# Optimization experiments

Hardware: AMD Instinct MI355X
Metric: run time of the kernel (lower is better)

## Reference

```python
import jax, jax.numpy as jnp
import numpy as np

D_MODEL = 1024
N_HEADS = 16
D_HEAD = D_MODEL // N_HEADS


def setup_inputs() -> dict:
    key = jax.random.key(0)
    ks = jax.random.split(key, 9)
    s = 1.0 / np.sqrt(D_MODEL)
    def lin(kw, kb):
        W = jax.random.uniform(kw, (D_MODEL, D_MODEL), jnp.float32, -s, s)
        b = jax.random.uniform(kb, (D_MODEL,), jnp.float32, -s, s)
        return W, b
    Wq, bq = lin(ks[0], ks[1])
    Wk, bk = lin(ks[2], ks[3])
    Wv, bv = lin(ks[4], ks[5])
    Wo, bo = lin(ks[6], ks[7])
    x = jax.random.normal(ks[8], (4, 2048, D_MODEL), jnp.float32)
    return {"x": x, "Wq": Wq, "bq": bq, "Wk": Wk, "bk": bk,
            "Wv": Wv, "bv": bv, "Wo": Wo, "bo": bo}


def reference(x, Wq, bq, Wk, bk, Wv, bv, Wo, bo):
    B, T, C = x.shape
    # torch Linear: y = x @ W.T + b
    Q = x @ Wq.T + bq
    K = x @ Wk.T + bk
    V = x @ Wv.T + bv
    # [B, H, T, Dh]
    Q = Q.reshape(B, T, N_HEADS, D_HEAD).transpose(0, 2, 1, 3)
    K = K.reshape(B, T, N_HEADS, D_HEAD).transpose(0, 2, 1, 3)
    V = V.reshape(B, T, N_HEADS, D_HEAD).transpose(0, 2, 1, 3)
    scale = jnp.float32(np.sqrt(D_HEAD))
    scores = jnp.einsum('bhqd,bhkd->bhqk', Q, K) / scale
    causal = jnp.tril(jnp.ones((T, T), dtype=bool))  # True where allowed
    scores = jnp.where(causal, scores, jnp.float32(-jnp.inf))
    attn = jax.nn.softmax(scores, axis=-1)
    out = jnp.einsum('bhqk,bhkd->bhqd', attn, V)
    out = out.transpose(0, 2, 1, 3).reshape(B, T, C)
    return out @ Wo.T + bo
```

## Files before the change

### kernel.cpp

```cpp
#include <hip/hip_runtime.h>
#include <hip/hip_bf16.h>


typedef float f32x4 __attribute__((ext_vector_type(4)));
typedef __bf16 bf16x8 __attribute__((ext_vector_type(8)));

#define DEVI __device__ __forceinline__

#define QSCALE 0.1803368801111204f

template<int N> struct IC { static constexpr int value = N; };

DEVI ushort f2b(float x) {
  __hip_bfloat16 h = __float2bfloat16(x);
  return __builtin_bit_cast(ushort, h);
}

DEVI unsigned int pkbf(float a, float b) {
#if __has_builtin(__builtin_amdgcn_cvt_pk_bf16_f32)
  typedef __bf16 bf16x2 __attribute__((ext_vector_type(2)));
  bf16x2 r = __builtin_amdgcn_cvt_pk_bf16_f32(a, b);
  return __builtin_bit_cast(unsigned int, r);
#else
  return (unsigned int)f2b(a) | ((unsigned int)f2b(b) << 16);
#endif
}

DEVI bf16x8 ldsFrag(const ushort* p) {
  return __builtin_bit_cast(bf16x8, *(const uint4*)p);
}

DEVI f32x4 mfma16(bf16x8 a, bf16x8 b, f32x4 c) {
  return __builtin_amdgcn_mfma_f32_16x16x32_bf16(a, b, c, 0, 0, 0);
}

DEVI void gload_lds16(const ushort* g, ushort* l) {
  __builtin_amdgcn_global_load_lds(
      (const __attribute__((address_space(1))) unsigned int*)g,
      (__attribute__((address_space(3))) unsigned int*)l, 16, 0, 0);
}

__global__ void k_cvt(const float4* __restrict__ in, ushort4* __restrict__ out, int n4) {
  int i = blockIdx.x * 256 + threadIdx.x;
  if (i >= n4) return;
  float4 f = in[i];
  ushort4 o;
  o.x = f2b(f.x); o.y = f2b(f.y); o.z = f2b(f.z); o.w = f2b(f.w);
  out[i] = o;
}

__global__ void k_cvtW(const float4* __restrict__ w0, const float4* __restrict__ w1,
                       const float4* __restrict__ w2, const float4* __restrict__ w3,
                       ushort4* __restrict__ out) {
  const int y = blockIdx.y;
  const float4* src = (y == 0) ? w0 : (y == 1) ? w1 : (y == 2) ? w2 : w3;
  const int i = blockIdx.x * 256 + threadIdx.x;
  float4 f = src[i];
  ushort4 o;
  o.x = f2b(f.x); o.y = f2b(f.y); o.z = f2b(f.z); o.w = f2b(f.w);
  out[y * 262144 + i] = o;
}

template<int MODE>
__global__ __launch_bounds__(256)
void k_gemm(const ushort* __restrict__ A, const ushort* __restrict__ W,
            const float* __restrict__ b0, const float* __restrict__ b1,
            const float* __restrict__ b2, float* __restrict__ outF,
            ushort* __restrict__ oQ, ushort* __restrict__ oK, ushort* __restrict__ oV) {
  __shared__ ushort As[128 * 32];
  __shared__ ushort Bs[128 * 32];
  const int tid = threadIdx.x;
  const int wave = tid >> 6, lane = tid & 63;
  const int col = lane & 15, quad = lane >> 4;
  const int id = blockIdx.x;
  const int s_ = id >> 3;
  const int m0 = ((id & 7) * 8 + (s_ & 7)) * 128;
  const int n0 = (s_ >> 3) * 128;
  const int wm = (wave >> 1) * 64, wn = (wave & 1) * 64;
  f32x4 acc[4][4] = {};

  const int srow = wave * 16 + (lane >> 2);
  const int scol = (lane & 3) * 8;
  const ushort* Ag = A + (m0 + srow) * 1024 + scol;
  const ushort* Wg = W + (n0 + srow) * 1024 + scol;
  ushort* AsBase0 = &As[(wave * 16) * 32];
  ushort* AsBase1 = &As[(64 + wave * 16) * 32];
  ushort* BsBase0 = &Bs[(wave * 16) * 32];
  ushort* BsBase1 = &Bs[(64 + wave * 16) * 32];

  const int matId = (MODE == 0) ? (n0 >> 10) : 0;

  auto kloop = [&](auto swc) {
    constexpr bool SW = (decltype(swc)::value != 0);
    for (int k0 = 0; k0 < 1024; k0 += 32) {
      __syncthreads();
      gload_lds16(Ag + k0,             AsBase0);
      gload_lds16(Ag + 64 * 1024 + k0, AsBase1);
      gload_lds16(Wg + k0,             BsBase0);
      gload_lds16(Wg + 64 * 1024 + k0, BsBase1);
      __syncthreads();

      bf16x8 af[4], bfr[4];
#pragma unroll
      for (int i = 0; i < 4; ++i)
        af[i] = ldsFrag(&As[(wm + i * 16 + col) * 32 + quad * 8]);
#pragma unroll
      for (int j = 0; j < 4; ++j)
        bfr[j] = ldsFrag(&Bs[(wn + j * 16 + col) * 32 + quad * 8]);
#pragma unroll
      for (int i = 0; i < 4; ++i)
#pragma unroll
        for (int j = 0; j < 4; ++j) {
          if constexpr (SW)
            acc[i][j] = mfma16(bfr[j], af[i], acc[i][j]);
          else
            acc[i][j] = mfma16(af[i], bfr[j], acc[i][j]);
        }
    }
  };

  if (MODE == 1 || matId < 2) kloop(IC<1>{}); else kloop(IC<0>{});

  if (MODE == 1) {
#pragma unroll
    for (int j = 0; j < 4; ++j) {
      const int nb = n0 + wn + j * 16 + quad * 4;
      const float4 bb = *(const float4*)&b0[nb];
#pragma unroll
      for (int i = 0; i < 4; ++i) {
        const int m = m0 + wm + i * 16 + col;
        float4 v;
        v.x = acc[i][j][0] + bb.x;
        v.y = acc[i][j][1] + bb.y;
        v.z = acc[i][j][2] + bb.z;
        v.w = acc[i][j][3] + bb.w;
        *(float4*)&outF[(size_t)m * 1024 + nb] = v;
      }
    }
  } else if (matId < 2) {
    ushort* dst = (matId == 0) ? oQ : oK;
    const float* bias = (matId == 0) ? b0 : b1;
    const float sc = (matId == 0) ? QSCALE : 1.0f;
#pragma unroll
    for (int j = 0; j < 4; ++j) {
      const int nl = ((n0 & 1023) + wn + j * 16 + quad * 4);
      const int h = nl >> 6, dh0 = nl & 63;
      const float4 bb = *(const float4*)&bias[nl];
#pragma unroll
      for (int i = 0; i < 4; ++i) {
        const int m = m0 + wm + i * 16 + col;
        const int b = m >> 11, t = m & 2047;
        ushort4 pk;
        pk.x = f2b((acc[i][j][0] + bb.x) * sc);
        pk.y = f2b((acc[i][j][1] + bb.y) * sc);
        pk.z = f2b((acc[i][j][2] + bb.z) * sc);
        pk.w = f2b((acc[i][j][3] + bb.w) * sc);
        *(ushort4*)&dst[(((size_t)(b * 16 + h) * 2048) + t) * 64 + dh0] = pk;
      }
    }
  } else {
#pragma unroll
    for (int j = 0; j < 4; ++j) {
      const int nl = ((n0 & 1023) + wn + j * 16 + col);
      const int h = nl >> 6, dh = nl & 63;
      const float bn = b2[nl];
#pragma unroll
      for (int i = 0; i < 4; ++i) {
        const int mBase = m0 + wm + i * 16 + quad * 4;
        const int b = mBase >> 11, t = mBase & 2047;
        ushort4 pk;
        pk.x = f2b(acc[i][j][0] + bn);
        pk.y = f2b(acc[i][j][1] + bn);
        pk.z = f2b(acc[i][j][2] + bn);
        pk.w = f2b(acc[i][j][3] + bn);
        *(ushort4*)&oV[(((size_t)(b * 16 + h) * 64) + dh) * 2048 + t] = pk;
      }
    }
  }
}

__global__ __launch_bounds__(256, 2)
void k_attn(const ushort* __restrict__ Q, const ushort* __restrict__ K,
            const ushort* __restrict__ Vt, ushort* __restrict__ AO) {
  __shared__ ushort Ks[2 * 4096];
  __shared__ ushort Vs[2 * 4096];
  __shared__ ushort Os[512];
  __shared__ ushort Ps[4 * 2 * 16 * 72];
  const int tid = threadIdx.x;
  const int wave = tid >> 6, lane = tid & 63;
  const int col = lane & 15, quad = lane >> 4;
  const int id = blockIdx.x;
  const int bh = (id & 7) * 8 + ((id >> 3) & 7);
  const int pr = id >> 6;
  const ushort* Qg = Q + (size_t)bh * 2048 * 64;
  const ushort* Kg = K + (size_t)bh * 2048 * 64;
  const ushort* Vg = Vt + (size_t)bh * 64 * 2048;

  if (tid < 128) {
    const ushort one = 0x3F80;
    ushort4 zv;
    if (tid < 8) { zv.x = one; zv.y = one; zv.z = one; zv.w = one; }
    else         { zv.x = 0;   zv.y = 0;   zv.z = 0;   zv.w = 0;   }
    *(ushort4*)&Os[tid * 4] = zv;
  }

  const int srow = wave * 16 + (lane >> 2);
  const int scol = (lane & 3) * 8;
  ushort* Pw0 = &Ps[((wave * 2 + 0) * 16 + col) * 72];
  ushort* Pw1 = &Ps[((wave * 2 + 1) * 16 + col) * 72];

  for (int pp = 0; pp < 2; ++pp) {
    const int t = pp ? (15 - pr) : pr;
    const int q0 = t * 128;

    bf16x8 qf[2][2];
#pragma unroll
    for (int s = 0; s < 2; ++s) {
      const ushort* p = Qg + (q0 + wave * 32 + s * 16 + col) * 64 + quad * 8;
      qf[s][0] = __builtin_bit_cast(bf16x8, *(const uint4*)p);
      qf[s][1] = __builtin_bit_cast(bf16x8, *(const uint4*)(p + 32));
    }

    f32x4 o[2][4] = {};
    f32x4 la[2] = {};

    const ushort* kPtr = Kg + srow * 64 + scol;
    const ushort* vPtr = Vg + srow * 2048 + scol;

    auto stage = [&](auto bufc) {
      constexpr int BUF = decltype(bufc)::value;
      ushort* kb = &Ks[BUF * 4096 + (wave * 16) * 32];
      ushort* vb = &Vs[BUF * 4096 + (wave * 16) * 32];
      gload_lds16(kPtr,      kb);
      gload_lds16(kPtr + 32, kb + 2048);
      gload_lds16(vPtr,      vb);
      gload_lds16(vPtr + 32, vb + 2048);
      kPtr += 64 * 64;
      vPtr += 64;
    };

    auto step = [&](auto bufc, auto maskc, int j0) {
      constexpr int BUF = decltype(bufc)::value;
      constexpr bool MASKED = (decltype(maskc)::value != 0);
      const ushort* Kb = &Ks[BUF * 4096];
      const ushort* Vb = &Vs[BUF * 4096];
      bf16x8 kf[4][2];
#pragma unroll
      for (int i = 0; i < 4; ++i) {
        kf[i][0] = ldsFrag(&Kb[(i * 16 + col) * 32 + quad * 8]);
        kf[i][1] = ldsFrag(&Kb[(64 + i * 16 + col) * 32 + quad * 8]);
      }
#pragma unroll
      for (int s = 0; s < 2; ++s) {
        ushort* Pw = s ? Pw1 : Pw0;
        const int dlim = MASKED ? (q0 + wave * 32 + s * 16 + col - j0 - quad * 4) : 0;
#pragma unroll
        for (int i = 0; i < 4; ++i) {
          f32x4 z = {0.f, 0.f, 0.f, 0.f};
          f32x4 sv = mfma16(kf[i][0], qf[s][0], z);
          sv = mfma16(kf[i][1], qf[s][1], sv);
          if (MASKED) {
#pragma unroll
            for (int r = 0; r < 4; ++r)
              if (i * 16 + r > dlim) sv[r] = -1e30f;
          }
          f32x4 pv;
#pragma unroll
          for (int r = 0; r < 4; ++r) pv[r] = __builtin_amdgcn_exp2f(sv[r]);
          uint2 pk;
          pk.x = pkbf(pv[0], pv[1]);
          pk.y = pkbf(pv[2], pv[3]);
          *(uint2*)&Pw[i * 16 + quad * 4] = pk;
        }
      }
      bf16x8 osf = ldsFrag(&Os[col * 32 + quad * 8]);
#pragma unroll
      for (int c = 0; c < 2; ++c) {
        bf16x8 pb0 = ldsFrag(&Pw0[c * 32 + quad * 8]);
        bf16x8 pb1 = ldsFrag(&Pw1[c * 32 + quad * 8]);
        la[0] = mfma16(osf, pb0, la[0]);
        la[1] = mfma16(osf, pb1, la[1]);
#pragma unroll
        for (int i = 0; i < 4; ++i) {
          bf16x8 vf = ldsFrag(&Vb[c * 2048 + (i * 16 + col) * 32 + quad * 8]);
          o[0][i] = mfma16(vf, pb0, o[0][i]);
          o[1][i] = mfma16(vf, pb1, o[1][i]);
        }
      }
    };

    __syncthreads();
    stage(IC<0>{});
    for (int it2 = 0; it2 < t; ++it2) {
      __syncthreads();
      stage(IC<1>{});
      step(IC<0>{}, IC<0>{}, 0);
      __syncthreads();
      stage(IC<0>{});
      step(IC<1>{}, IC<0>{}, 0);
    }
    __syncthreads();
    stage(IC<1>{});
    step(IC<0>{}, IC<1>{}, q0);
    __syncthreads();
    step(IC<1>{}, IC<1>{}, q0 + 64);

    const float invs[2] = {1.0f / __shfl(la[0][0], col), 1.0f / __shfl(la[1][0], col)};
    const int b = bh >> 4, h = bh & 15;
#pragma unroll
    for (int s = 0; s < 2; ++s) {
      const float inv = invs[s];
      const int tq = q0 + wave * 32 + s * 16 + col;
      ushort* dst = AO + (size_t)(b * 2048 + tq) * 1024 + h * 64;
#pragma unroll
      for (int i = 0; i < 4; ++i) {
        f32x4 v = o[s][i];
        ushort4 pk;
        pk.x = f2b(v[0] * inv);
        pk.y = f2b(v[1] * inv);
        pk.z = f2b(v[2] * inv);
        pk.w = f2b(v[3] * inv);
        *(ushort4*)&dst[i * 16 + quad * 4] = pk;
      }
    }
  }
}

extern "C" void kernel_launch(void* const* d_in, const int* in_sizes, int n_in,
                              void* d_out, int out_size, void* d_ws, size_t ws_size,
                              hipStream_t stream) {
  const float* x  = (const float*)d_in[0];
  const float* Wq = (const float*)d_in[1];
  const float* bq = (const float*)d_in[2];
  const float* Wk = (const float*)d_in[3];
  const float* bk = (const float*)d_in[4];
  const float* Wv = (const float*)d_in[5];
  const float* bv = (const float*)d_in[6];
  const float* Wo = (const float*)d_in[7];
  const float* bo = (const float*)d_in[8];
  float* out = (float*)d_out;

  char* ws = (char*)d_ws;
  ushort* xb    = (ushort*)ws;
  ushort* Wcat  = (ushort*)(ws + (size_t)16 * 1024 * 1024);
  ushort* Wob   = Wcat + (size_t)3 * 1024 * 1024;
  ushort* Qh    = (ushort*)(ws + (size_t)24 * 1024 * 1024);
  ushort* Kh    = Qh + (size_t)8192 * 1024;
  ushort* Vt    = Kh + (size_t)8192 * 1024;
  ushort* AO    = Vt + (size_t)8192 * 1024;

  k_cvt<<<8192, 256, 0, stream>>>((const float4*)x, (ushort4*)xb, 8192 * 1024 / 4);
  k_cvtW<<<dim3(1024, 4), 256, 0, stream>>>((const float4*)Wq, (const float4*)Wk,
                                            (const float4*)Wv, (const float4*)Wo,
                                            (ushort4*)Wcat);

  k_gemm<0><<<1536, 256, 0, stream>>>(xb, Wcat, bq, bk, bv, nullptr, Qh, Kh, Vt);

  k_attn<<<512, 256, 0, stream>>>(Qh, Kh, Vt, AO);

  k_gemm<1><<<512, 256, 0, stream>>>(AO, Wob, bo, nullptr, nullptr, out,
                                     nullptr, nullptr, nullptr);
}
```

Baseline: 262.8 us.

## Swizzle LDS tiles with BK=64 in GEMM and split attention into per-tile blocks

The GEMM now stages 64-wide K slices into LDS using an XOR-swizzled row layout, which halves the number of barriers per K loop and avoids LDS bank conflicts on fragment reads. The attention kernel uses the same swizzled 64-column K/V layout. It also launches one block per query tile instead of pairing two tiles per block, with an interleaved tile order to balance the causal work. Occupancy hints rise to three blocks per CU. GEMM LDS use doubles and the attention kernel loses the balanced pairing, so more blocks have uneven causal lengths.

After: 253.7 us. 3.5% less time.

```diff
diff --git a/kernel.cpp b/kernel.cpp
--- a/kernel.cpp
+++ b/kernel.cpp
@@ -67,8 +67,8 @@
             const float* __restrict__ b0, const float* __restrict__ b1,
             const float* __restrict__ b2, float* __restrict__ outF,
             ushort* __restrict__ oQ, ushort* __restrict__ oK, ushort* __restrict__ oV) {
-  __shared__ ushort As[128 * 32];
-  __shared__ ushort Bs[128 * 32];
+  __shared__ ushort As[128 * 64];
+  __shared__ ushort Bs[128 * 64];
   const int tid = threadIdx.x;
   const int wave = tid >> 6, lane = tid & 63;
   const int col = lane & 15, quad = lane >> 4;
@@ -79,43 +79,45 @@
   const int wm = (wave >> 1) * 64, wn = (wave & 1) * 64;
   f32x4 acc[4][4] = {};
 
-  const int srow = wave * 16 + (lane >> 2);
-  const int scol = (lane & 3) * 8;
-  const ushort* Ag = A + (m0 + srow) * 1024 + scol;
-  const ushort* Wg = W + (n0 + srow) * 1024 + scol;
-  ushort* AsBase0 = &As[(wave * 16) * 32];
-  ushort* AsBase1 = &As[(64 + wave * 16) * 32];
-  ushort* BsBase0 = &Bs[(wave * 16) * 32];
-  ushort* BsBase1 = &Bs[(64 + wave * 16) * 32];
+  const int grow = lane >> 3;
+  const int gchunk = ((lane & 7) ^ grow) * 8;
+  const ushort* Ag = A + (size_t)(m0 + wave * 8 + grow) * 1024 + gchunk;
+  const ushort* Wg = W + (size_t)(n0 + wave * 8 + grow) * 1024 + gchunk;
+  ushort* AsW = &As[wave * 512];
+  ushort* BsW = &Bs[wave * 512];
 
   const int matId = (MODE == 0) ? (n0 >> 10) : 0;
+  const int cswz = col & 7;
 
   auto kloop = [&](auto swc) {
     constexpr bool SW = (decltype(swc)::value != 0);
-    for (int k0 = 0; k0 < 1024; k0 += 32) {
+    for (int k0 = 0; k0 < 1024; k0 += 64) {
       __syncthreads();
-      gload_lds16(Ag + k0,             AsBase0);
-      gload_lds16(Ag + 64 * 1024 + k0, AsBase1);
-      gload_lds16(Wg + k0,             BsBase0);
-      gload_lds16(Wg + 64 * 1024 + k0, BsBase1);
+#pragma unroll
+      for (int g = 0; g < 4; ++g) {
+        gload_lds16(Ag + (size_t)g * 32 * 1024 + k0, AsW + g * 2048);
+        gload_lds16(Wg + (size_t)g * 32 * 1024 + k0, BsW + g * 2048);
+      }
       __syncthreads();
-
-      bf16x8 af[4], bfr[4];
-#pragma unroll
-      for (int i = 0; i < 4; ++i)
-        af[i] = ldsFrag(&As[(wm + i * 16 + col) * 32 + quad * 8]);
-#pragma unroll
-      for (int j = 0; j < 4; ++j)
-        bfr[j] = ldsFrag(&Bs[(wn + j * 16 + col) * 32 + quad * 8]);
-#pragma unroll
-      for (int i = 0; i < 4; ++i)
-#pragma unroll
-        for (int j = 0; j < 4; ++j) {
-          if constexpr (SW)
-            acc[i][j] = mfma16(bfr[j], af[i], acc[i][j]);
-          else
-            acc[i][j] = mfma16(af[i], bfr[j], acc[i][j]);
-        }
+#pragma unroll
+      for (int kk = 0; kk < 2; ++kk) {
+        bf16x8 af[4], bfr[4];
+#pragma unroll
+        for (int i = 0; i < 4; ++i)
+          af[i] = ldsFrag(&As[(wm + i * 16 + col) * 64 + (((kk * 4 + quad) ^ cswz) * 8)]);
+#pragma unroll
+        for (int j = 0; j < 4; ++j)
+          bfr[j] = ldsFrag(&Bs[(wn + j * 16 + col) * 64 + (((kk * 4 + quad) ^ cswz) * 8)]);
+#pragma unroll
+        for (int i = 0; i < 4; ++i)
+#pragma unroll
+          for (int j = 0; j < 4; ++j) {
+            if constexpr (SW)
+              acc[i][j] = mfma16(bfr[j], af[i], acc[i][j]);
+            else
+              acc[i][j] = mfma16(af[i], bfr[j], acc[i][j]);
+          }
+      }
     }
   };
 
@@ -179,7 +181,7 @@
   }
 }
 
-__global__ __launch_bounds__(256, 2)
+__global__ __launch_bounds__(256, 3)
 void k_attn(const ushort* __restrict__ Q, const ushort* __restrict__ K,
             const ushort* __restrict__ Vt, ushort* __restrict__ AO) {
   __shared__ ushort Ks[2 * 4096];
@@ -191,7 +193,10 @@
   const int col = lane & 15, quad = lane >> 4;
   const int id = blockIdx.x;
   const int bh = (id & 7) * 8 + ((id >> 3) & 7);
-  const int pr = id >> 6;
+  const int tt = id >> 6;
+  const int hi = tt >> 2, lo = tt & 3;
+  const int t = (hi & 1) ? (15 - (hi >> 1) - 2 * lo) : ((hi >> 1) + 2 * lo);
+  const int q0 = t * 128;
   const ushort* Qg = Q + (size_t)bh * 2048 * 64;
   const ushort* Kg = K + (size_t)bh * 2048 * 64;
   const ushort* Vg = Vt + (size_t)bh * 64 * 2048;
@@ -204,124 +209,119 @@
     *(ushort4*)&Os[tid * 4] = zv;
   }
 
-  const int srow = wave * 16 + (lane >> 2);
-  const int scol = (lane & 3) * 8;
+  bf16x8 qf[2][2];
+#pragma unroll
+  for (int s = 0; s < 2; ++s) {
+    const ushort* p = Qg + (q0 + wave * 32 + s * 16 + col) * 64 + quad * 8;
+    qf[s][0] = __builtin_bit_cast(bf16x8, *(const uint4*)p);
+    qf[s][1] = __builtin_bit_cast(bf16x8, *(const uint4*)(p + 32));
+  }
+
+  f32x4 o[2][4] = {};
+  f32x4 la[2] = {};
+
+  const int grow = lane >> 3;
+  const int gchunk = ((lane & 7) ^ grow) * 8;
+  const ushort* kPtr = Kg + (wave * 8 + grow) * 64 + gchunk;
+  const ushort* vPtr = Vg + (size_t)(wave * 8 + grow) * 2048 + gchunk;
   ushort* Pw0 = &Ps[((wave * 2 + 0) * 16 + col) * 72];
   ushort* Pw1 = &Ps[((wave * 2 + 1) * 16 + col) * 72];
-
-  for (int pp = 0; pp < 2; ++pp) {
-    const int t = pp ? (15 - pr) : pr;
-    const int q0 = t * 128;
-
-    bf16x8 qf[2][2];
+  const int cswz = col & 7;
+
+  auto stage = [&](auto bufc) {
+    constexpr int BUF = decltype(bufc)::value;
+    ushort* kb = &Ks[BUF * 4096 + wave * 512];
+    ushort* vb = &Vs[BUF * 4096 + wave * 512];
+    gload_lds16(kPtr,             kb);
+    gload_lds16(kPtr + 32 * 64,   kb + 2048);
+    gload_lds16(vPtr,             vb);
+    gload_lds16(vPtr + 32 * 2048, vb + 2048);
+    kPtr += 64 * 64;
+    vPtr += 64;
+  };
+
+  auto step = [&](auto bufc, auto maskc, int j0) {
+    constexpr int BUF = decltype(bufc)::value;
+    constexpr bool MASKED = (decltype(maskc)::value != 0);
+    const ushort* Kb = &Ks[BUF * 4096];
+    const ushort* Vb = &Vs[BUF * 4096];
+    bf16x8 kf[4][2];
+#pragma unroll
+    for (int i = 0; i < 4; ++i) {
+      kf[i][0] = ldsFrag(&Kb[(i * 16 + col) * 64 + (((0 * 4 + quad) ^ cswz) * 8)]);
+      kf[i][1] = ldsFrag(&Kb[(i * 16 + col) * 64 + (((1 * 4 + quad) ^ cswz) * 8)]);
+    }
 #pragma unroll
     for (int s = 0; s < 2; ++s) {
-      const ushort* p = Qg + (q0 + wave * 32 + s * 16 + col) * 64 + quad * 8;
-      qf[s][0] = __builtin_bit_cast(bf16x8, *(const uint4*)p);
-      qf[s][1] = __builtin_bit_cast(bf16x8, *(const uint4*)(p + 32));
-    }
-
-    f32x4 o[2][4] = {};
-    f32x4 la[2] = {};
-
-    const ushort* kPtr = Kg + srow * 64 + scol;
-    const ushort* vPtr = Vg + srow * 2048 + scol;
-
-    auto stage = [&](auto bufc) {
-      constexpr int BUF = decltype(bufc)::value;
-      ushort* kb = &Ks[BUF * 4096 + (wave * 16) * 32];
-      ushort* vb = &Vs[BUF * 4096 + (wave * 16) * 32];
-      gload_lds16(kPtr,      kb);
-      gload_lds16(kPtr + 32, kb + 2048);
-      gload_lds16(vPtr,      vb);
-      gload_lds16(vPtr + 32, vb + 2048);
-      kPtr += 64 * 64;
-      vPtr += 64;
-    };
-
-    auto step = [&](auto bufc, auto maskc, int j0) {
-      constexpr int BUF = decltype(bufc)::value;
-      constexpr bool MASKED = (decltype(maskc)::value != 0);
-      const ushort* Kb = &Ks[BUF * 4096];
-      const ushort* Vb = &Vs[BUF * 4096];
-      bf16x8 kf[4][2];
-#pragma unroll
-      for (int i = 0; i < 4; ++i) {
-        kf[i][0] = ldsFrag(&Kb[(i * 16 + col) * 32 + quad * 8]);
-        kf[i][1] = ldsFrag(&Kb[(64 + i * 16 + col) * 32 + quad * 8]);
-      }
-#pragma unroll
-      for (int s = 0; s < 2; ++s) {
-        ushort* Pw = s ? Pw1 : Pw0;
-        const int dlim = MASKED ? (q0 + wave * 32 + s * 16 + col - j0 - quad * 4) : 0;
-#pragma unroll
-        for (int i = 0; i < 4; ++i) {
-          f32x4 z = {0.f, 0.f, 0.f, 0.f};
-          f32x4 sv = mfma16(kf[i][0], qf[s][0], z);
-          sv = mfma16(kf[i][1], qf[s][1], sv);
-          if (MASKED) {
-#pragma unroll
-            for (int r = 0; r < 4; ++r)
-              if (i * 16 + r > dlim) sv[r] = -1e30f;
-          }
-          f32x4 pv;
-#pragma unroll
-          for (int r = 0; r < 4; ++r) pv[r] = __builtin_amdgcn_exp2f(sv[r]);
-          uint2 pk;
-          pk.x = pkbf(pv[0], pv[1]);
-          pk.y = pkbf(pv[2], pv[3]);
-          *(uint2*)&Pw[i * 16 + quad * 4] = pk;
+      ushort* Pw = s ? Pw1 : Pw0;
+      const int dlim = MASKED ? (q0 + wave * 32 + s * 16 + col - j0 - quad * 4) : 0;
+#pragma unroll
+      for (int i = 0; i < 4; ++i) {
+        f32x4 z = {0.f, 0.f, 0.f, 0.f};
+        f32x4 sv = mfma16(kf[i][0], qf[s][0], z);
+        sv = mfma16(kf[i][1], qf[s][1], sv);
+        if (MASKED) {
+#pragma unroll
+          for (int r = 0; r < 4; ++r)
+            if (i * 16 + r > dlim) sv[r] = -1e30f;
         }
-      }
-      bf16x8 osf = ldsFrag(&Os[col * 32 + quad * 8]);
-#pragma unroll
-      for (int c = 0; c < 2; ++c) {
-        bf16x8 pb0 = ldsFrag(&Pw0[c * 32 + quad * 8]);
-        bf16x8 pb1 = ldsFrag(&Pw1[c * 32 + quad * 8]);
-        la[0] = mfma16(osf, pb0, la[0]);
-        la[1] = mfma16(osf, pb1, la[1]);
-#pragma unroll
-        for (int i = 0; i < 4; ++i) {
-          bf16x8 vf = ldsFrag(&Vb[c * 2048 + (i * 16 + col) * 32 + quad * 8]);
-          o[0][i] = mfma16(vf, pb0, o[0][i]);
-          o[1][i] = mfma16(vf, pb1, o[1][i]);
-        }
-      }
-    };
-
+        f32x4 pv;
+#pragma unroll
+        for (int r = 0; r < 4; ++r) pv[r] = __builtin_amdgcn_exp2f(sv[r]);
+        uint2 pk;
+        pk.x = pkbf(pv[0], pv[1]);
+        pk.y = pkbf(pv[2], pv[3]);
+        *(uint2*)&Pw[i * 16 + quad * 4] = pk;
+      }
+    }
+    bf16x8 osf = ldsFrag(&Os[col * 32 + quad * 8]);
+#pragma unroll
+    for (int c = 0; c < 2; ++c) {
+      bf16x8 pb0 = ldsFrag(&Pw0[c * 32 + quad * 8]);
+      bf16x8 pb1 = ldsFrag(&Pw1[c * 32 + quad * 8]);
+      la[0] = mfma16(osf, pb0, la[0]);
+      la[1] = mfma16(osf, pb1, la[1]);
+#pragma unroll
+      for (int i = 0; i < 4; ++i) {
+        bf16x8 vf = ldsFrag(&Vb[(i * 16 + col) * 64 + (((c * 4 + quad) ^ cswz) * 8)]);
+        o[0][i] = mfma16(vf, pb0, o[0][i]);
+        o[1][i] = mfma16(vf, pb1, o[1][i]);
+      }
+    }
+  };
+
+  __syncthreads();
+  stage(IC<0>{});
+  for (int it2 = 0; it2 < t; ++it2) {
+    __syncthreads();
+    stage(IC<1>{});
+    step(IC<0>{}, IC<0>{}, 0);
     __syncthreads();
     stage(IC<0>{});
-    for (int it2 = 0; it2 < t; ++it2) {
-      __syncthreads();
-      stage(IC<1>{});
-      step(IC<0>{}, IC<0>{}, 0);
-      __syncthreads();
-      stage(IC<0>{});
-      step(IC<1>{}, IC<0>{}, 0);
-    }
-    __syncthreads();
-    stage(IC<1>{});
-    step(IC<0>{}, IC<1>{}, q0);
-    __syncthreads();
-    step(IC<1>{}, IC<1>{}, q0 + 64);
-
-    const float invs[2] = {1.0f / __shfl(la[0][0], col), 1.0f / __shfl(la[1][0], col)};
-    const int b = bh >> 4, h = bh & 15;
-#pragma unroll
-    for (int s = 0; s < 2; ++s) {
-      const float inv = invs[s];
-      const int tq = q0 + wave * 32 + s * 16 + col;
-      ushort* dst = AO + (size_t)(b * 2048 + tq) * 1024 + h * 64;
-#pragma unroll
-      for (int i = 0; i < 4; ++i) {
-        f32x4 v = o[s][i];
-        ushort4 pk;
-        pk.x = f2b(v[0] * inv);
-        pk.y = f2b(v[1] * inv);
-        pk.z = f2b(v[2] * inv);
-        pk.w = f2b(v[3] * inv);
-        *(ushort4*)&dst[i * 16 + quad * 4] = pk;
-      }
+    step(IC<1>{}, IC<0>{}, 0);
+  }
+  __syncthreads();
+  stage(IC<1>{});
+  step(IC<0>{}, IC<1>{}, q0);
+  __syncthreads();
+  step(IC<1>{}, IC<1>{}, q0 + 64);
+
+  const float invs[2] = {1.0f / __shfl(la[0][0], col), 1.0f / __shfl(la[1][0], col)};
+  const int b = bh >> 4, h = bh & 15;
+#pragma unroll
+  for (int s = 0; s < 2; ++s) {
+    const float inv = invs[s];
+    const int tq = q0 + wave * 32 + s * 16 + col;
+    ushort* dst = AO + (size_t)(b * 2048 + tq) * 1024 + h * 64;
+#pragma unroll
+    for (int i = 0; i < 4; ++i) {
+      f32x4 v = o[s][i];
+      ushort4 pk;
+      pk.x = f2b(v[0] * inv);
+      pk.y = f2b(v[1] * inv);
+      pk.z = f2b(v[2] * inv);
+      pk.w = f2b(v[3] * inv);
+      *(ushort4*)&dst[i * 16 + quad * 4] = pk;
     }
   }
 }
@@ -356,7 +356,7 @@
 
   k_gemm<0><<<1536, 256, 0, stream>>>(xb, Wcat, bq, bk, bv, nullptr, Qh, Kh, Vt);
 
-  k_attn<<<512, 256, 0, stream>>>(Qh, Kh, Vt, AO);
+  k_attn<<<1024, 256, 0, stream>>>(Qh, Kh, Vt, AO);
 
   k_gemm<1><<<512, 256, 0, stream>>>(AO, Wob, bo, nullptr, nullptr, out,
                                      nullptr, nullptr, nullptr);
```
